# Performance work log

Hardware: AMD Instinct MI355X
Metric: run time of the kernel (lower is better)

Reference implementation:

```python
import jax, jax.numpy as jnp
import numpy as np

B, S, F = 32, 8, 4
N0, N1, N2 = 2048, 4096, 2048
H, OUT = 1024, 256
IN = N0 + N1 + N2  # 8192
SC_LAYERS = 2


def setup_inputs() -> dict:
    key = jax.random.key(0)
    ks = jax.random.split(key, 16)
    rn = jax.random.normal
    inp = {
        'xs0': rn(ks[0], (B, S, N0), jnp.float32),
        'xs1': rn(ks[1], (B, S, N1), jnp.float32),
        'xs2': rn(ks[2], (B, S, N2), jnp.float32),
        # dense Laplacians, scaled so L@x keeps unit-ish variance
        'L0': rn(ks[3], (N0, N0), jnp.float32) / np.sqrt(N0).astype(np.float32),
        'L1': rn(ks[4], (N1, N1), jnp.float32) / np.sqrt(N1).astype(np.float32),
        'L2': rn(ks[5], (N2, N2), jnp.float32) / np.sqrt(N2).astype(np.float32),
        # per-layer, per-filter diagonal weights (std=0.01 as in torch init)
        'Wc0': 0.01 * rn(ks[6], (SC_LAYERS, F, N0), jnp.float32),
        'Wc1': 0.01 * rn(ks[7], (SC_LAYERS, F, N1), jnp.float32),
        'Wc2': 0.01 * rn(ks[8], (SC_LAYERS, F, N2), jnp.float32),
        # MLP params (xavier-ish)
        'W_in': rn(ks[9], (IN, H), jnp.float32) / np.sqrt(IN).astype(np.float32),
        'b_in': jnp.zeros((H,), jnp.float32),
        'W_h': rn(ks[10], (H, H), jnp.float32) / np.sqrt(H).astype(np.float32),
        'b_h': jnp.zeros((H,), jnp.float32),
        'W_out': rn(ks[11], (H, OUT), jnp.float32) / np.sqrt(H).astype(np.float32),
        'b_out': jnp.zeros((OUT,), jnp.float32),
    }
    return inp


def _conv_stack(x, L, Wc):
    # x: [B, S, n]; L: [n, n]; Wc: [layers, F, n]
    for l in range(Wc.shape[0]):
        # batched Laplacian matmul: (L @ x_bs) for every (b, s)
        Lx = jnp.einsum('bsn,mn->bsm', x, L)  # [B, S, n]
        # diagonal filter scaling + activation + sum over filters (fused)
        x = jax.nn.relu(Lx[:, :, None, :] * Wc[l][None, None, :, :]).sum(axis=2)
    return x


def reference(xs0, xs1, xs2, L0, L1, L2, Wc0, Wc1, Wc2,
              W_in, b_in, W_h, b_h, W_out, b_out):
    h = jnp.concatenate([
        _conv_stack(xs0, L0, Wc0),
        _conv_stack(xs1, L1, Wc1),
        _conv_stack(xs2, L2, Wc2),
    ], axis=-1)                      # [B, S, IN]
    h = h.sum(axis=1)                # sum over sequence -> [B, IN]
    h = jax.nn.relu(h @ W_in + b_in)
    h = jax.nn.relu(h @ W_h + b_h)   # single hidden layer (nn_layers=2)
    return h @ W_out + b_out         # [B, OUT]
```

## Files before the change

### kernel.cpp

```cpp
#include <hip/hip_runtime.h>
#include <hip/hip_bf16.h>


#define B_    32
#define S_    8
#define BS_   256
#define F_    4
#define IN_   8192
#define H_    1024
#define OUT_  256

#define L_TOT  25165824LL
#define LOFF1  4194304LL
#define LOFF2  20971520LL

typedef __attribute__((ext_vector_type(8)))  short bf16x8;
typedef __attribute__((ext_vector_type(4)))  short short4v;
typedef __attribute__((ext_vector_type(8)))  short short8v;
typedef __attribute__((ext_vector_type(16))) float f32x16;

typedef const __attribute__((address_space(1))) void* gas_ptr;
typedef __attribute__((address_space(3))) void* las_ptr;

__device__ __forceinline__ void gload16(const void* g, void* s) {
    __builtin_amdgcn_global_load_lds((gas_ptr)g, (las_ptr)s, 16, 0, 0);
}

__device__ __forceinline__ unsigned short rne_bf16(float f) {
    unsigned int u = __builtin_bit_cast(unsigned int, f);
    u += 0x7FFFu + ((u >> 16) & 1u);
    return (unsigned short)(u >> 16);
}

__global__ void k_pre(const float* __restrict__ L0, const float* __restrict__ L1,
                      const float* __restrict__ L2, unsigned short* __restrict__ Lb,
                      const float* __restrict__ x0, const float* __restrict__ x1,
                      const float* __restrict__ x2,
                      unsigned short* __restrict__ Xhi, unsigned short* __restrict__ Xlo,
                      const float* __restrict__ Wc0, const float* __restrict__ Wc1,
                      const float* __restrict__ Wc2, float* __restrict__ PM)
{
    const int bx = blockIdx.x, tid = threadIdx.x;
    if (bx < 3072) {
        const long long b0 = (long long)bx * 8192;
        const float* src; long long off;
        if (b0 < LOFF1)      { src = L0; off = 0; }
        else if (b0 < LOFF2) { src = L1; off = LOFF1; }
        else                 { src = L2; off = LOFF2; }
        const float* p2 = src + (b0 - off) + tid * 8;
        float4 va[4], vb[4];
        #pragma unroll
        for (int j = 0; j < 4; ++j) {
            va[j] = *(const float4*)(p2 + j * 2048);
            vb[j] = *(const float4*)(p2 + j * 2048 + 4);
        }
        #pragma unroll
        for (int j = 0; j < 4; ++j) {
            short8v o;
            o[0] = (short)rne_bf16(va[j].x); o[1] = (short)rne_bf16(va[j].y);
            o[2] = (short)rne_bf16(va[j].z); o[3] = (short)rne_bf16(va[j].w);
            o[4] = (short)rne_bf16(vb[j].x); o[5] = (short)rne_bf16(vb[j].y);
            o[6] = (short)rne_bf16(vb[j].z); o[7] = (short)rne_bf16(vb[j].w);
            *(short8v*)(Lb + b0 + j * 2048 + tid * 8) = o;
        }
    } else if (bx < 3584) {
        const int base = (bx - 3072) * 4096 + tid * 8;
        #pragma unroll
        for (int u = 0; u < 2; ++u) {
            int e = base + u * 2048;
            int m = e >> 13, c = e & 8191;
            const float* src; int n, c0;
            if (c < 2048)      { src = x0; n = 2048; c0 = c; }
            else if (c < 6144) { src = x1; n = 4096; c0 = c - 2048; }
            else               { src = x2; n = 2048; c0 = c - 6144; }
            const float* p = src + (size_t)m * n + c0;
            float4 a = *(const float4*)(p);
            float4 b = *(const float4*)(p + 4);
            float v[8] = {a.x, a.y, a.z, a.w, b.x, b.y, b.z, b.w};
            short8v h, l;
            #pragma unroll
            for (int i = 0; i < 8; ++i) {
                unsigned short hb = rne_bf16(v[i]);
                float hf = __builtin_bit_cast(float, (unsigned int)hb << 16);
                h[i] = (short)hb;
                l[i] = (short)rne_bf16(v[i] - hf);
            }
            *(short8v*)(Xhi + (size_t)m * IN_ + c) = h;
            *(short8v*)(Xlo + (size_t)m * IN_ + c) = l;
        }
    } else {
        const int base = (bx - 3584) * 2048 + tid * 8;
        #pragma unroll
        for (int i = 0; i < 8; ++i) {
            int idx = base + i;
            int l = idx / IN_, n = idx % IN_;
            const float* Wc; int nb, j;
            if (n < 2048)      { Wc = Wc0; nb = 2048; j = n;        }
            else if (n < 6144) { Wc = Wc1; nb = 4096; j = n - 2048; }
            else               { Wc = Wc2; nb = 2048; j = n - 6144; }
            float p = 0.f, m = 0.f;
            #pragma unroll
            for (int f = 0; f < F_; ++f) {
                float w = Wc[(l * F_ + f) * nb + j];
                p += fmaxf(w, 0.f);
                m += fmaxf(-w, 0.f);
            }
            PM[(l * 2 + 0) * IN_ + n] = p;
            PM[(l * 2 + 1) * IN_ + n] = m;
        }
    }
}

__global__ __launch_bounds__(256, 2) void k_gemm(
    const unsigned short* __restrict__ Xhi, const unsigned short* __restrict__ Xlo,
    const unsigned short* __restrict__ Lb,
    float* __restrict__ pf)
{
    __shared__ __attribute__((aligned(16))) unsigned short Ah[3][128 * 32];
    __shared__ __attribute__((aligned(16))) unsigned short Al[3][128 * 32];
    __shared__ __attribute__((aligned(16))) unsigned short Bs[3][128 * 32];

    const int bx = blockIdx.x;
    int n_, noff, mt, nt, sk, k0, iters; long long loff;
    if (bx < 256) {
        sk = bx & 3; int v = bx >> 2; mt = v & 1; nt = v >> 1;
        n_ = 4096; noff = 2048; loff = LOFF1; k0 = sk << 10; iters = 32;
    } else {
        int u = bx - 256;
        if (u < 128) { sk = u & 3; int v = u >> 2; mt = v & 1; nt = v >> 1;
                       n_ = 2048; noff = 0; loff = 0; }
        else { u -= 128; sk = u & 3; int v = u >> 2; mt = v & 1; nt = v >> 1;
                       n_ = 2048; noff = 6144; loff = LOFF2; }
        k0 = sk << 9; iters = 16;
    }

    const int tid = threadIdx.x;

    const int sg = ((tid & 3) ^ ((tid >> 3) & 3)) << 3;
    const unsigned short* gAh = Xhi + (size_t)(mt * 128 + (tid >> 2)) * IN_ + noff + k0 + sg;
    const unsigned short* gAl = Xlo + (size_t)(mt * 128 + (tid >> 2)) * IN_ + noff + k0 + sg;
    const unsigned short* gB  = Lb + loff + (size_t)(nt * 128 + (tid >> 2)) * n_ + k0 + sg;
    const size_t a64 = (size_t)64 * IN_, b64 = (size_t)64 * n_;
    const int tb = tid * 16;

    char *aC = (char*)&Ah[0][0], *aN = (char*)&Ah[1][0], *aS = (char*)&Ah[2][0];
    char *lC = (char*)&Al[0][0], *lN = (char*)&Al[1][0], *lS = (char*)&Al[2][0];
    char *bC = (char*)&Bs[0][0], *bN = (char*)&Bs[1][0], *bS = (char*)&Bs[2][0];

    #define STAGE(pA, pL, pB, ko)                                  \
        do {                                                       \
            gload16(gAh + (ko),       (pA) + tb);                  \
            gload16(gAh + (ko) + a64, (pA) + 4096 + tb);           \
            gload16(gAl + (ko),       (pL) + tb);                  \
            gload16(gAl + (ko) + a64, (pL) + 4096 + tb);           \
            gload16(gB + (ko),        (pB) + tb);                  \
            gload16(gB + (ko) + b64,  (pB) + 4096 + tb);           \
        } while (0)

    const int l = tid & 63, w = tid >> 6;
    const int l31 = l & 31, lh = l >> 5;
    const int wm = w >> 1, wn = w & 1;
    const int swz = (l31 >> 1) & 3;
    const int ar0 = (wm * 64 + l31) * 32, ar1 = ar0 + 1024;
    const int br0 = (wn * 64 + l31) * 32, br1 = br0 + 1024;

    f32x16 a00, a01, a10, a11;
    #pragma unroll
    for (int r = 0; r < 16; ++r) { a00[r] = 0.f; a01[r] = 0.f; a10[r] = 0.f; a11[r] = 0.f; }

    STAGE(aC, lC, bC, 0);
    STAGE(aN, lN, bN, 32);

    for (int it = 0; it < iters; ++it) {
        if (it < iters - 1) asm volatile("s_waitcnt vmcnt(6)" ::: "memory");
        else                asm volatile("s_waitcnt vmcnt(0)" ::: "memory");
        __builtin_amdgcn_s_barrier();
        asm volatile("" ::: "memory");

        if (it + 2 < iters) STAGE(aS, lS, bS, (it + 2) * 32);
        __builtin_amdgcn_sched_barrier(0);

        const unsigned short* cA = (const unsigned short*)aC;
        const unsigned short* cL = (const unsigned short*)lC;
        const unsigned short* cB = (const unsigned short*)bC;
        #pragma unroll
        for (int t = 0; t < 2; ++t) {
            const int sidx = (((t << 1) + lh) ^ swz) << 3;
            bf16x8 fah0 = *(const bf16x8*)&cA[ar0 + sidx];
            bf16x8 fah1 = *(const bf16x8*)&cA[ar1 + sidx];
            bf16x8 fal0 = *(const bf16x8*)&cL[ar0 + sidx];
            bf16x8 fal1 = *(const bf16x8*)&cL[ar1 + sidx];
            bf16x8 fb0  = *(const bf16x8*)&cB[br0 + sidx];
            bf16x8 fb1  = *(const bf16x8*)&cB[br1 + sidx];
            a00 = __builtin_amdgcn_mfma_f32_32x32x16_bf16(fal0, fb0, a00, 0, 0, 0);
            a00 = __builtin_amdgcn_mfma_f32_32x32x16_bf16(fah0, fb0, a00, 0, 0, 0);
            a01 = __builtin_amdgcn_mfma_f32_32x32x16_bf16(fal0, fb1, a01, 0, 0, 0);
            a01 = __builtin_amdgcn_mfma_f32_32x32x16_bf16(fah0, fb1, a01, 0, 0, 0);
            a10 = __builtin_amdgcn_mfma_f32_32x32x16_bf16(fal1, fb0, a10, 0, 0, 0);
            a10 = __builtin_amdgcn_mfma_f32_32x32x16_bf16(fah1, fb0, a10, 0, 0, 0);
            a11 = __builtin_amdgcn_mfma_f32_32x32x16_bf16(fal1, fb1, a11, 0, 0, 0);
            a11 = __builtin_amdgcn_mfma_f32_32x32x16_bf16(fah1, fb1, a11, 0, 0, 0);
        }
        asm volatile("" ::: "memory");

        char* t1 = aC; aC = aN; aN = aS; aS = t1;
        char* t2 = lC; lC = lN; lN = lS; lS = t2;
        char* t3 = bC; bC = bN; bN = bS; bS = t3;
    }
    #undef STAGE

    const int colg = noff + nt * 128 + wn * 64 + l31;
    #pragma unroll
    for (int rb = 0; rb < 2; ++rb) {
        float* po = pf + ((size_t)sk * 256 + mt * 128 + wm * 64 + rb * 32 + 4 * lh) * IN_;
        const f32x16& c0 = rb ? a10 : a00;
        const f32x16& c1 = rb ? a11 : a01;
        #pragma unroll
        for (int e = 0; e < 16; ++e) {
            const int row = (e & 3) + 8 * (e >> 2);
            po[(size_t)row * IN_ + colg]      = c0[e];
            po[(size_t)row * IN_ + colg + 32] = c1[e];
        }
    }
}

__global__ void k_epi0(const float* __restrict__ pf,
                       const float* __restrict__ Pv, const float* __restrict__ Mv,
                       unsigned short* __restrict__ Yhi, unsigned short* __restrict__ Ylo) {
    int e = (blockIdx.x * 256 + threadIdx.x) * 4;
    int m = e >> 13, c = e & 8191;
    const float* p0 = pf + (size_t)m * IN_ + c;
    float vs[4] = {0.f, 0.f, 0.f, 0.f};
    #pragma unroll
    for (int s = 0; s < 4; ++s) {
        float4 v = *(const float4*)(p0 + (size_t)s * 256 * IN_);
        vs[0] += v.x; vs[1] += v.y; vs[2] += v.z; vs[3] += v.w;
    }
    float4 pv = *(const float4*)(Pv + c);
    float4 mv = *(const float4*)(Mv + c);
    float pa[4] = {pv.x, pv.y, pv.z, pv.w};
    float ma[4] = {mv.x, mv.y, mv.z, mv.w};
    short hv[4], lv[4];
    #pragma unroll
    for (int j = 0; j < 4; ++j) {
        float y = fmaxf(vs[j], 0.f) * pa[j] + fmaxf(-vs[j], 0.f) * ma[j];
        unsigned short hb = rne_bf16(y);
        float hf = __builtin_bit_cast(float, (unsigned int)hb << 16);
        hv[j] = (short)hb;
        lv[j] = (short)rne_bf16(y - hf);
    }
    short4v h = {hv[0], hv[1], hv[2], hv[3]};
    short4v lo = {lv[0], lv[1], lv[2], lv[3]};
    *(short4v*)(Yhi + (size_t)m * IN_ + c) = h;
    *(short4v*)(Ylo + (size_t)m * IN_ + c) = lo;
}

__global__ void k_epi1s(const float* __restrict__ pf,
                        const float* __restrict__ Pv, const float* __restrict__ Mv,
                        float* __restrict__ hsum) {
    int e = (blockIdx.x * 256 + threadIdx.x) * 4;
    int b = e >> 13, c = e & 8191;
    float4 pv = *(const float4*)(Pv + c);
    float4 mv = *(const float4*)(Mv + c);
    float pa[4] = {pv.x, pv.y, pv.z, pv.w};
    float ma[4] = {mv.x, mv.y, mv.z, mv.w};
    float hs[4] = {0.f, 0.f, 0.f, 0.f};
    for (int q = 0; q < 8; ++q) {
        const int m = b * 8 + q;
        const float* p0 = pf + (size_t)m * IN_ + c;
        float vs[4] = {0.f, 0.f, 0.f, 0.f};
        #pragma unroll
        for (int s = 0; s < 4; ++s) {
            float4 v = *(const float4*)(p0 + (size_t)s * 256 * IN_);
            vs[0] += v.x; vs[1] += v.y; vs[2] += v.z; vs[3] += v.w;
        }
        #pragma unroll
        for (int j = 0; j < 4; ++j)
            hs[j] += fmaxf(vs[j], 0.f) * pa[j] + fmaxf(-vs[j], 0.f) * ma[j];
    }
    *(float4*)(hsum + (size_t)b * IN_ + c) = *(float4*)hs;
}

template<int KC>
__global__ __launch_bounds__(256) void k_mlp3(
    const float* __restrict__ X, const float* __restrict__ W,
    float* __restrict__ P, int K, int H)
{
    __shared__ float Xs[32][KC];
    const int tid = threadIdx.x;
    const int lane = tid & 63;
    const int mg = tid >> 6;
    const int h = (blockIdx.x * 64 + lane) * 4;
    const int c = blockIdx.y, k0 = c * KC;

    for (int i = tid * 4; i < 32 * KC; i += 1024) {
        int m = i / KC, kk = i % KC;
        *(float4*)&Xs[m][kk] = *(const float4*)(X + (size_t)m * K + k0 + kk);
    }
    __syncthreads();

    float4 acc[8];
    #pragma unroll
    for (int m = 0; m < 8; ++m) acc[m] = {0.f, 0.f, 0.f, 0.f};

    const float* wp = W + (size_t)k0 * H + h;
    for (int kk = 0; kk < KC; kk += 4) {
        float4 w4[4];
        #pragma unroll
        for (int u = 0; u < 4; ++u)
            w4[u] = *(const float4*)(wp + (size_t)(kk + u) * H);
        #pragma unroll
        for (int m = 0; m < 8; ++m) {
            float4 xv = *(const float4*)&Xs[mg * 8 + m][kk];
            acc[m].x = fmaf(xv.x, w4[0].x, acc[m].x);
            acc[m].y = fmaf(xv.x, w4[0].y, acc[m].y);
            acc[m].z = fmaf(xv.x, w4[0].z, acc[m].z);
            acc[m].w = fmaf(xv.x, w4[0].w, acc[m].w);
            acc[m].x = fmaf(xv.y, w4[1].x, acc[m].x);
            acc[m].y = fmaf(xv.y, w4[1].y, acc[m].y);
            acc[m].z = fmaf(xv.y, w4[1].z, acc[m].z);
            acc[m].w = fmaf(xv.y, w4[1].w, acc[m].w);
            acc[m].x = fmaf(xv.z, w4[2].x, acc[m].x);
            acc[m].y = fmaf(xv.z, w4[2].y, acc[m].y);
            acc[m].z = fmaf(xv.z, w4[2].z, acc[m].z);
            acc[m].w = fmaf(xv.z, w4[2].w, acc[m].w);
            acc[m].x = fmaf(xv.w, w4[3].x, acc[m].x);
            acc[m].y = fmaf(xv.w, w4[3].y, acc[m].y);
            acc[m].z = fmaf(xv.w, w4[3].z, acc[m].z);
            acc[m].w = fmaf(xv.w, w4[3].w, acc[m].w);
        }
    }
    #pragma unroll
    for (int m = 0; m < 8; ++m)
        *(float4*)(P + ((size_t)c * 32 + mg * 8 + m) * H + h) = acc[m];
}

__global__ void k_reduce4(const float* __restrict__ P, const float* __restrict__ bias,
                          float* __restrict__ Y, int NC, int MH4, int H, int do_relu) {
    int idx = blockIdx.x * 256 + threadIdx.x;
    if (idx >= MH4) return;
    int h0 = (idx * 4) % H;
    float4 s = *(const float4*)(bias + h0);
    for (int c = 0; c < NC; ++c) {
        float4 v = *(const float4*)(P + (size_t)c * MH4 * 4 + (size_t)idx * 4);
        s.x += v.x; s.y += v.y; s.z += v.z; s.w += v.w;
    }
    if (do_relu) {
        s.x = fmaxf(s.x, 0.f); s.y = fmaxf(s.y, 0.f);
        s.z = fmaxf(s.z, 0.f); s.w = fmaxf(s.w, 0.f);
    }
    *(float4*)(Y + (size_t)idx * 4) = s;
}

extern "C" void kernel_launch(void* const* d_in, const int* in_sizes, int n_in,
                              void* d_out, int out_size, void* d_ws, size_t ws_size,
                              hipStream_t stream) {
    const float* xs0  = (const float*)d_in[0];
    const float* xs1  = (const float*)d_in[1];
    const float* xs2  = (const float*)d_in[2];
    const float* L0   = (const float*)d_in[3];
    const float* L1   = (const float*)d_in[4];
    const float* L2   = (const float*)d_in[5];
    const float* Wc0  = (const float*)d_in[6];
    const float* Wc1  = (const float*)d_in[7];
    const float* Wc2  = (const float*)d_in[8];
    const float* W_in = (const float*)d_in[9];
    const float* b_in = (const float*)d_in[10];
    const float* W_h  = (const float*)d_in[11];
    const float* b_h  = (const float*)d_in[12];
    const float* W_out= (const float*)d_in[13];
    const float* b_out= (const float*)d_in[14];

    char* w = (char*)d_ws;
    float*          PM  = (float*)w;          w += (size_t)4 * IN_ * 4;
    unsigned short* Lb  = (unsigned short*)w; w += (size_t)L_TOT * 2;
    unsigned short* Xhi = (unsigned short*)w; w += (size_t)BS_ * IN_ * 2;
    unsigned short* Xlo = (unsigned short*)w; w += (size_t)BS_ * IN_ * 2;
    unsigned short* Yhi = (unsigned short*)w; w += (size_t)BS_ * IN_ * 2;
    unsigned short* Ylo = (unsigned short*)w; w += (size_t)BS_ * IN_ * 2;
    float*          pf  = (float*)w;          w += (size_t)4 * BS_ * IN_ * 4;
    float*          hsum= (float*)w;          w += (size_t)32 * IN_ * 4;
    float*          p1  = pf;
    float*          h1  = (float*)w;          w += (size_t)32 * H_ * 4;
    float*          p2  = (float*)w;          w += (size_t)32 * 32 * H_ * 4;
    float*          h2  = (float*)w;          w += (size_t)32 * H_ * 4;
    float*          p3  = (float*)w;          w += (size_t)32 * 32 * OUT_ * 4;

    k_pre<<<3592, 256, 0, stream>>>(L0, L1, L2, Lb, xs0, xs1, xs2, Xhi, Xlo,
                                    Wc0, Wc1, Wc2, PM);

    k_gemm<<<512, 256, 0, stream>>>(Xhi, Xlo, Lb, pf);
    k_epi0<<<2048, 256, 0, stream>>>(pf, PM + 0 * IN_, PM + 1 * IN_, Yhi, Ylo);
    k_gemm<<<512, 256, 0, stream>>>(Yhi, Ylo, Lb, pf);
    k_epi1s<<<256, 256, 0, stream>>>(pf, PM + 2 * IN_, PM + 3 * IN_, hsum);

    {
        dim3 g(4, 128);
        k_mlp3<64><<<g, 256, 0, stream>>>(hsum, W_in, p1, IN_, H_);
        k_reduce4<<<32, 256, 0, stream>>>(p1, b_in, h1, 128, 8192, H_, 1);
    }
    {
        dim3 g(4, 32);
        k_mlp3<32><<<g, 256, 0, stream>>>(h1, W_h, p2, H_, H_);
        k_reduce4<<<32, 256, 0, stream>>>(p2, b_h, h2, 32, 8192, H_, 1);
    }
    {
        dim3 g(1, 32);
        k_mlp3<32><<<g, 256, 0, stream>>>(h2, W_out, p3, H_, OUT_);
        k_reduce4<<<8, 256, 0, stream>>>(p3, b_out, (float*)d_out, 32, 2048, OUT_, 0);
    }
}
```

Before: 211.9 us.

## Use nontemporal loads in prep, interleave GEMM block types, raise MFMA priority

The prep kernel now reads the fp32 Laplacians and inputs with nontemporal loads, so the one-shot streaming reads do not pollute the cache. GEMM blocks are interleaved so that long (n=4096, 32-iteration) and short (16-iteration) tiles alternate in block order, which should balance load across CUs instead of running all long blocks first. The MFMA section is wrapped in s_setprio so waves issuing matrix ops get scheduling priority over waves issuing loads. Each change is small and carries little risk to correctness.

```diff
diff --git a/kernel.cpp b/kernel.cpp
--- a/kernel.cpp
+++ b/kernel.cpp
@@ -18,6 +18,7 @@
 typedef __attribute__((ext_vector_type(4)))  short short4v;
 typedef __attribute__((ext_vector_type(8)))  short short8v;
 typedef __attribute__((ext_vector_type(16))) float f32x16;
+typedef __attribute__((ext_vector_type(4)))  float f32x4;
 
 typedef const __attribute__((address_space(1))) void* gas_ptr;
 typedef __attribute__((address_space(3))) void* las_ptr;
@@ -47,21 +48,18 @@
         if (b0 < LOFF1)      { src = L0; off = 0; }
         else if (b0 < LOFF2) { src = L1; off = LOFF1; }
         else                 { src = L2; off = LOFF2; }
-        const float* p2 = src + (b0 - off) + tid * 8;
-        float4 va[4], vb[4];
-        #pragma unroll
-        for (int j = 0; j < 4; ++j) {
-            va[j] = *(const float4*)(p2 + j * 2048);
-            vb[j] = *(const float4*)(p2 + j * 2048 + 4);
-        }
-        #pragma unroll
-        for (int j = 0; j < 4; ++j) {
+        const float* pb = src + (b0 - off) + tid * 8;
+        #pragma unroll
+        for (int u = 0; u < 4; ++u) {
+            const float* p = pb + u * 2048;
+            f32x4 a = __builtin_nontemporal_load((const f32x4*)p);
+            f32x4 b = __builtin_nontemporal_load((const f32x4*)p + 1);
             short8v o;
-            o[0] = (short)rne_bf16(va[j].x); o[1] = (short)rne_bf16(va[j].y);
-            o[2] = (short)rne_bf16(va[j].z); o[3] = (short)rne_bf16(va[j].w);
-            o[4] = (short)rne_bf16(vb[j].x); o[5] = (short)rne_bf16(vb[j].y);
-            o[6] = (short)rne_bf16(vb[j].z); o[7] = (short)rne_bf16(vb[j].w);
-            *(short8v*)(Lb + b0 + j * 2048 + tid * 8) = o;
+            o[0] = (short)rne_bf16(a.x); o[1] = (short)rne_bf16(a.y);
+            o[2] = (short)rne_bf16(a.z); o[3] = (short)rne_bf16(a.w);
+            o[4] = (short)rne_bf16(b.x); o[5] = (short)rne_bf16(b.y);
+            o[6] = (short)rne_bf16(b.z); o[7] = (short)rne_bf16(b.w);
+            *(short8v*)(Lb + b0 + u * 2048 + tid * 8) = o;
         }
     } else if (bx < 3584) {
         const int base = (bx - 3072) * 4096 + tid * 8;
@@ -74,8 +72,8 @@
             else if (c < 6144) { src = x1; n = 4096; c0 = c - 2048; }
             else               { src = x2; n = 2048; c0 = c - 6144; }
             const float* p = src + (size_t)m * n + c0;
-            float4 a = *(const float4*)(p);
-            float4 b = *(const float4*)(p + 4);
+            f32x4 a = __builtin_nontemporal_load((const f32x4*)p);
+            f32x4 b = __builtin_nontemporal_load((const f32x4*)p + 1);
             float v[8] = {a.x, a.y, a.z, a.w, b.x, b.y, b.z, b.w};
             short8v h, l;
             #pragma unroll
@@ -121,16 +119,16 @@
     __shared__ __attribute__((aligned(16))) unsigned short Bs[3][128 * 32];
 
     const int bx = blockIdx.x;
+    const int idx = bx >> 1;
     int n_, noff, mt, nt, sk, k0, iters; long long loff;
-    if (bx < 256) {
-        sk = bx & 3; int v = bx >> 2; mt = v & 1; nt = v >> 1;
+    if ((bx & 1) == 0) {
+        sk = idx & 3; int v = idx >> 2; mt = v & 1; nt = v >> 1;
         n_ = 4096; noff = 2048; loff = LOFF1; k0 = sk << 10; iters = 32;
     } else {
-        int u = bx - 256;
-        if (u < 128) { sk = u & 3; int v = u >> 2; mt = v & 1; nt = v >> 1;
-                       n_ = 2048; noff = 0; loff = 0; }
-        else { u -= 128; sk = u & 3; int v = u >> 2; mt = v & 1; nt = v >> 1;
-                       n_ = 2048; noff = 6144; loff = LOFF2; }
+        if (idx < 128) { int u = idx;       sk = u & 3; int v = u >> 2; mt = v & 1; nt = v >> 1;
+                         n_ = 2048; noff = 0; loff = 0; }
+        else           { int u = idx - 128; sk = u & 3; int v = u >> 2; mt = v & 1; nt = v >> 1;
+                         n_ = 2048; noff = 6144; loff = LOFF2; }
         k0 = sk << 9; iters = 16;
     }
 
@@ -183,6 +181,7 @@
         const unsigned short* cA = (const unsigned short*)aC;
         const unsigned short* cL = (const unsigned short*)lC;
         const unsigned short* cB = (const unsigned short*)bC;
+        __builtin_amdgcn_s_setprio(1);
         #pragma unroll
         for (int t = 0; t < 2; ++t) {
             const int sidx = (((t << 1) + lh) ^ swz) << 3;
@@ -201,6 +200,7 @@
             a11 = __builtin_amdgcn_mfma_f32_32x32x16_bf16(fal1, fb1, a11, 0, 0, 0);
             a11 = __builtin_amdgcn_mfma_f32_32x32x16_bf16(fah1, fb1, a11, 0, 0, 0);
         }
+        __builtin_amdgcn_s_setprio(0);
         asm volatile("" ::: "memory");
 
         char* t1 = aC; aC = aN; aN = aS; aS = t1;
```

Result: no change. 207.9 us (-1.9%).
